# Kernel optimization log

Measured on AMD Instinct MI355X. Metric: run time of the kernel, lower is better.

Reference implementation:

```python
import jax, jax.numpy as jnp
import numpy as np

T = 1_000_000      # number of feature rows
D = 82             # STSIM feature dim (hardcoded Linear(82, 1))
NUM_GROUPS = 256   # N = mask.max() + 1 in the original (fixed for jit)


def setup_inputs() -> dict:
    key = jax.random.key(0)
    k1, k2, k3, k4, k5 = jax.random.split(key, 5)
    X1 = jax.random.normal(k1, (T, D), jnp.float32)
    X2 = jax.random.normal(k2, (T, D), jnp.float32)
    Y = jax.random.normal(k3, (T,), jnp.float32)
    mask = jax.random.randint(k4, (T,), 0, NUM_GROUPS)
    # Linear(82,1,bias=False) weight; positive (matches init_weight = 1/var)
    # so sqrt(M((X1-X2)^2)) is real.
    W = jax.random.uniform(k5, (1, D), jnp.float32, 0.01, 1.0)
    return {"X1": X1, "X2": X2, "Y": Y, "W": W, "mask": mask}


def _criterion(x, Y, mask):
    # Vectorized version of the per-group Pearson-correlation loop:
    # one pass of segment reductions instead of N full-array boolean masks.
    seg = lambda v: jax.ops.segment_sum(v, mask, num_segments=NUM_GROUPS)
    counts = seg(jnp.ones_like(x))                      # [N]
    xc = x - (seg(x) / counts)[mask]                    # per-group centered
    yc = Y - (seg(Y) / counts)[mask]
    nom = seg(xc * yc)                                  # [N]
    denom = jnp.sqrt(seg(xc * xc) * seg(yc * yc))       # [N]
    return jnp.sum(jnp.abs(nom / denom)) / NUM_GROUPS


def reference(X1, X2, Y, W, mask):
    # pred = sqrt(Linear((X1 - X2)^2))  -> [T, 1]
    pred = jnp.sqrt(((X1 - X2) ** 2) @ W.T)
    coeff = _criterion(pred[:, 0], Y, mask)
    return coeff, pred
```

## Files before the change

### kernel.cpp

```cpp
#include <hip/hip_runtime.h>
#include <hip/hip_bf16.h>

#define T_ROWS 1000000
#define D 82
#define NG 256

#define WS_CNT   0
#define WS_SUMP  256
#define WS_SUMY  512
#define WS_MEANP 768
#define WS_MEANY 1024
#define WS_SXY   1280
#define WS_SXX   1536
#define WS_SYY   1792
#define WS_FLOATS 2048

__global__ __launch_bounds__(256) void pred_kernel(
    const float* __restrict__ X1, const float* __restrict__ X2,
    const float* __restrict__ Y, const float* __restrict__ W,
    const int* __restrict__ mask, float* __restrict__ pred_out,
    float* __restrict__ ws)
{
    __shared__ float lds_w[D];
    __shared__ float lds_cnt[NG], lds_sp[NG], lds_sy[NG];
    const int t = threadIdx.x;
    if (t < D) lds_w[t] = W[t];
    lds_cnt[t] = 0.f; lds_sp[t] = 0.f; lds_sy[t] = 0.f;
    __syncthreads();

    const int pair = blockIdx.x * 256 + t;
    if (pair < T_ROWS / 2) {
        const float4* __restrict__ p1 = (const float4*)(X1 + (size_t)pair * (2 * D));
        const float4* __restrict__ p2 = (const float4*)(X2 + (size_t)pair * (2 * D));
        float accA = 0.f, accB = 0.f;
        #pragma unroll 5
        for (int k = 0; k < 20; ++k) {
            float4 a = p1[k], b = p2[k];
            float d;
            d = a.x - b.x; accA += d * d * lds_w[4 * k + 0];
            d = a.y - b.y; accA += d * d * lds_w[4 * k + 1];
            d = a.z - b.z; accA += d * d * lds_w[4 * k + 2];
            d = a.w - b.w; accA += d * d * lds_w[4 * k + 3];
        }
        {
            float4 a = p1[20], b = p2[20];
            float d;
            d = a.x - b.x; accA += d * d * lds_w[80];
            d = a.y - b.y; accA += d * d * lds_w[81];
            d = a.z - b.z; accB += d * d * lds_w[0];
            d = a.w - b.w; accB += d * d * lds_w[1];
        }
        #pragma unroll 5
        for (int k = 21; k < 41; ++k) {
            float4 a = p1[k], b = p2[k];
            const int c = 4 * k - 82;
            float d;
            d = a.x - b.x; accB += d * d * lds_w[c + 0];
            d = a.y - b.y; accB += d * d * lds_w[c + 1];
            d = a.z - b.z; accB += d * d * lds_w[c + 2];
            d = a.w - b.w; accB += d * d * lds_w[c + 3];
        }
        const float pA = sqrtf(accA);
        const float pB = sqrtf(accB);
        pred_out[2 * pair]     = pA;
        pred_out[2 * pair + 1] = pB;

        const int2   gg = *(const int2*)(mask + 2 * (size_t)pair);
        const float2 yy = *(const float2*)(Y + 2 * (size_t)pair);
        atomicAdd(&lds_cnt[gg.x], 1.f);  atomicAdd(&lds_cnt[gg.y], 1.f);
        atomicAdd(&lds_sp[gg.x], pA);    atomicAdd(&lds_sp[gg.y], pB);
        atomicAdd(&lds_sy[gg.x], yy.x);  atomicAdd(&lds_sy[gg.y], yy.y);
    }
    __syncthreads();
    atomicAdd(&ws[WS_CNT  + t], lds_cnt[t]);
    atomicAdd(&ws[WS_SUMP + t], lds_sp[t]);
    atomicAdd(&ws[WS_SUMY + t], lds_sy[t]);
}

__global__ void means_kernel(float* __restrict__ ws)
{
    const int g = threadIdx.x;
    const float c = ws[WS_CNT + g];
    ws[WS_MEANP + g] = ws[WS_SUMP + g] / c;
    ws[WS_MEANY + g] = ws[WS_SUMY + g] / c;
}

__global__ __launch_bounds__(256) void corr_kernel(
    const float* __restrict__ pred, const float* __restrict__ Y,
    const int* __restrict__ mask, float* __restrict__ ws)
{
    __shared__ float mP[NG], mY[NG], sxy[NG], sxx[NG], syy[NG];
    const int t = threadIdx.x;
    mP[t] = ws[WS_MEANP + t];
    mY[t] = ws[WS_MEANY + t];
    sxy[t] = 0.f; sxx[t] = 0.f; syy[t] = 0.f;
    __syncthreads();

    const int stride = gridDim.x * blockDim.x;
    for (int r = blockIdx.x * blockDim.x + t; r < T_ROWS; r += stride) {
        const int g = mask[r];
        const float xc = pred[r] - mP[g];
        const float yc = Y[r]    - mY[g];
        atomicAdd(&sxy[g], xc * yc);
        atomicAdd(&sxx[g], xc * xc);
        atomicAdd(&syy[g], yc * yc);
    }
    __syncthreads();
    atomicAdd(&ws[WS_SXY + t], sxy[t]);
    atomicAdd(&ws[WS_SXX + t], sxx[t]);
    atomicAdd(&ws[WS_SYY + t], syy[t]);
}

__global__ void final_kernel(const float* __restrict__ ws, float* __restrict__ out)
{
    __shared__ float red[NG];
    const int g = threadIdx.x;
    const float r = ws[WS_SXY + g] / sqrtf(ws[WS_SXX + g] * ws[WS_SYY + g]);
    red[g] = fabsf(r);
    __syncthreads();
    for (int s = 128; s > 0; s >>= 1) {
        if (g < s) red[g] += red[g + s];
        __syncthreads();
    }
    if (g == 0) out[0] = red[0] / (float)NG;
}

extern "C" void kernel_launch(void* const* d_in, const int* in_sizes, int n_in,
                              void* d_out, int out_size, void* d_ws, size_t ws_size,
                              hipStream_t stream)
{
    const float* X1   = (const float*)d_in[0];
    const float* X2   = (const float*)d_in[1];
    const float* Y    = (const float*)d_in[2];
    const float* W    = (const float*)d_in[3];
    const int*   mask = (const int*)d_in[4];
    float* out = (float*)d_out;
    float* ws  = (float*)d_ws;

    hipMemsetAsync(ws, 0, WS_FLOATS * sizeof(float), stream);

    const int pairs = T_ROWS / 2;
    const int gridA = (pairs + 255) / 256;
    pred_kernel<<<gridA, 256, 0, stream>>>(X1, X2, Y, W, mask, out + 1, ws);
    means_kernel<<<1, 256, 0, stream>>>(ws);
    corr_kernel<<<1024, 256, 0, stream>>>(out + 1, Y, mask, ws);
    final_kernel<<<1, 256, 0, stream>>>(ws, out);
}
```

Before: 723.2 us.

## Fuse prediction and correlation into one pass using raw-moment sums

Replaces the two-pass centered correlation (pred, means, corr kernels) with a single fused kernel that accumulates count, sums, cross-products and squares per group. The final kernel computes the correlation from these raw moments in double. The fused kernel stages a 64-row tile of X1-X2 differences in LDS with coalesced float4 loads and splits each row's dot product across 4 threads. It removes a kernel launch and the second read of pred, Y and mask. In exchange it issues per-row global atomics with no LDS pre-aggregation, which could contend heavily on 256 groups, and the float raw-moment accumulation risks cancellation error.

```diff
diff --git a/kernel.cpp b/kernel.cpp
--- a/kernel.cpp
+++ b/kernel.cpp
@@ -4,119 +4,91 @@
 #define T_ROWS 1000000
 #define D 82
 #define NG 256
+#define ROWS_PER_BLOCK 64
+#define TILE_FLOATS (ROWS_PER_BLOCK * D)
+#define TILE_F4     (TILE_FLOATS / 4)
 
-#define WS_CNT   0
-#define WS_SUMP  256
-#define WS_SUMY  512
-#define WS_MEANP 768
-#define WS_MEANY 1024
-#define WS_SXY   1280
-#define WS_SXX   1536
-#define WS_SYY   1792
-#define WS_FLOATS 2048
+#define WS_CNT 0
+#define WS_SX  256
+#define WS_SY  512
+#define WS_SXY 768
+#define WS_SXX 1024
+#define WS_SYY 1280
+#define WS_FLOATS 1536
 
-__global__ __launch_bounds__(256) void pred_kernel(
+__global__ __launch_bounds__(256) void fused_kernel(
     const float* __restrict__ X1, const float* __restrict__ X2,
     const float* __restrict__ Y, const float* __restrict__ W,
     const int* __restrict__ mask, float* __restrict__ pred_out,
     float* __restrict__ ws)
 {
-    __shared__ float lds_w[D];
-    __shared__ float lds_cnt[NG], lds_sp[NG], lds_sy[NG];
+    __shared__ float s_diff[TILE_FLOATS];
+    __shared__ float s_w[D];
+    __shared__ float s_part[4][ROWS_PER_BLOCK];
+
     const int t = threadIdx.x;
-    if (t < D) lds_w[t] = W[t];
-    lds_cnt[t] = 0.f; lds_sp[t] = 0.f; lds_sy[t] = 0.f;
+    const size_t r0 = (size_t)blockIdx.x * ROWS_PER_BLOCK;
+    const size_t base = r0 * D;
+
+    const float4* __restrict__ a4 = (const float4*)(X1 + base);
+    const float4* __restrict__ b4 = (const float4*)(X2 + base);
+    float4* s4 = (float4*)s_diff;
+
+    for (int i = t; i < TILE_F4; i += 256) {
+        float4 a = a4[i];
+        float4 b = b4[i];
+        float4 d;
+        d.x = a.x - b.x; d.y = a.y - b.y; d.z = a.z - b.z; d.w = a.w - b.w;
+        s4[i] = d;
+    }
+    if (t < D) s_w[t] = W[t];
     __syncthreads();
 
-    const int pair = blockIdx.x * 256 + t;
-    if (pair < T_ROWS / 2) {
-        const float4* __restrict__ p1 = (const float4*)(X1 + (size_t)pair * (2 * D));
-        const float4* __restrict__ p2 = (const float4*)(X2 + (size_t)pair * (2 * D));
-        float accA = 0.f, accB = 0.f;
-        #pragma unroll 5
-        for (int k = 0; k < 20; ++k) {
-            float4 a = p1[k], b = p2[k];
-            float d;
-            d = a.x - b.x; accA += d * d * lds_w[4 * k + 0];
-            d = a.y - b.y; accA += d * d * lds_w[4 * k + 1];
-            d = a.z - b.z; accA += d * d * lds_w[4 * k + 2];
-            d = a.w - b.w; accA += d * d * lds_w[4 * k + 3];
-        }
-        {
-            float4 a = p1[20], b = p2[20];
-            float d;
-            d = a.x - b.x; accA += d * d * lds_w[80];
-            d = a.y - b.y; accA += d * d * lds_w[81];
-            d = a.z - b.z; accB += d * d * lds_w[0];
-            d = a.w - b.w; accB += d * d * lds_w[1];
-        }
-        #pragma unroll 5
-        for (int k = 21; k < 41; ++k) {
-            float4 a = p1[k], b = p2[k];
-            const int c = 4 * k - 82;
-            float d;
-            d = a.x - b.x; accB += d * d * lds_w[c + 0];
-            d = a.y - b.y; accB += d * d * lds_w[c + 1];
-            d = a.z - b.z; accB += d * d * lds_w[c + 2];
-            d = a.w - b.w; accB += d * d * lds_w[c + 3];
-        }
-        const float pA = sqrtf(accA);
-        const float pB = sqrtf(accB);
-        pred_out[2 * pair]     = pA;
-        pred_out[2 * pair + 1] = pB;
-
-        const int2   gg = *(const int2*)(mask + 2 * (size_t)pair);
-        const float2 yy = *(const float2*)(Y + 2 * (size_t)pair);
-        atomicAdd(&lds_cnt[gg.x], 1.f);  atomicAdd(&lds_cnt[gg.y], 1.f);
-        atomicAdd(&lds_sp[gg.x], pA);    atomicAdd(&lds_sp[gg.y], pB);
-        atomicAdd(&lds_sy[gg.x], yy.x);  atomicAdd(&lds_sy[gg.y], yy.y);
+    const int q = t >> 6;
+    const int row = t & 63;
+    const int start = (q < 2) ? q * 21 : 42 + (q - 2) * 20;
+    const int len = (q < 2) ? 21 : 20;
+    const float* __restrict__ dr = s_diff + row * D;
+    float acc = 0.f;
+    #pragma unroll 7
+    for (int j = 0; j < len; ++j) {
+        const int k = start + j;
+        const float d = dr[k];
+        acc += d * d * s_w[k];
     }
-    __syncthreads();
-    atomicAdd(&ws[WS_CNT  + t], lds_cnt[t]);
-    atomicAdd(&ws[WS_SUMP + t], lds_sp[t]);
-    atomicAdd(&ws[WS_SUMY + t], lds_sy[t]);
-}
-
-__global__ void means_kernel(float* __restrict__ ws)
-{
-    const int g = threadIdx.x;
-    const float c = ws[WS_CNT + g];
-    ws[WS_MEANP + g] = ws[WS_SUMP + g] / c;
-    ws[WS_MEANY + g] = ws[WS_SUMY + g] / c;
-}
-
-__global__ __launch_bounds__(256) void corr_kernel(
-    const float* __restrict__ pred, const float* __restrict__ Y,
-    const int* __restrict__ mask, float* __restrict__ ws)
-{
-    __shared__ float mP[NG], mY[NG], sxy[NG], sxx[NG], syy[NG];
-    const int t = threadIdx.x;
-    mP[t] = ws[WS_MEANP + t];
-    mY[t] = ws[WS_MEANY + t];
-    sxy[t] = 0.f; sxx[t] = 0.f; syy[t] = 0.f;
+    s_part[q][row] = acc;
     __syncthreads();
 
-    const int stride = gridDim.x * blockDim.x;
-    for (int r = blockIdx.x * blockDim.x + t; r < T_ROWS; r += stride) {
-        const int g = mask[r];
-        const float xc = pred[r] - mP[g];
-        const float yc = Y[r]    - mY[g];
-        atomicAdd(&sxy[g], xc * yc);
-        atomicAdd(&sxx[g], xc * xc);
-        atomicAdd(&syy[g], yc * yc);
+    if (t < ROWS_PER_BLOCK) {
+        const float s = s_part[0][t] + s_part[1][t] + s_part[2][t] + s_part[3][t];
+        const float p = sqrtf(s);
+        pred_out[r0 + t] = p;
+
+        const int g = mask[r0 + t];
+        const float y = Y[r0 + t];
+        atomicAdd(&ws[WS_CNT + g], 1.0f);
+        atomicAdd(&ws[WS_SX  + g], p);
+        atomicAdd(&ws[WS_SY  + g], y);
+        atomicAdd(&ws[WS_SXY + g], p * y);
+        atomicAdd(&ws[WS_SXX + g], p * p);
+        atomicAdd(&ws[WS_SYY + g], y * y);
     }
-    __syncthreads();
-    atomicAdd(&ws[WS_SXY + t], sxy[t]);
-    atomicAdd(&ws[WS_SXX + t], sxx[t]);
-    atomicAdd(&ws[WS_SYY + t], syy[t]);
 }
 
 __global__ void final_kernel(const float* __restrict__ ws, float* __restrict__ out)
 {
     __shared__ float red[NG];
     const int g = threadIdx.x;
-    const float r = ws[WS_SXY + g] / sqrtf(ws[WS_SXX + g] * ws[WS_SYY + g]);
-    red[g] = fabsf(r);
+    const double n   = (double)ws[WS_CNT + g];
+    const double sx  = (double)ws[WS_SX  + g];
+    const double sy  = (double)ws[WS_SY  + g];
+    const double sxy = (double)ws[WS_SXY + g];
+    const double sxx = (double)ws[WS_SXX + g];
+    const double syy = (double)ws[WS_SYY + g];
+    const double num  = n * sxy - sx * sy;
+    const double varx = n * sxx - sx * sx;
+    const double vary = n * syy - sy * sy;
+    red[g] = (float)fabs(num / sqrt(varx * vary));
     __syncthreads();
     for (int s = 128; s > 0; s >>= 1) {
         if (g < s) red[g] += red[g + s];
@@ -139,10 +111,7 @@
 
     hipMemsetAsync(ws, 0, WS_FLOATS * sizeof(float), stream);
 
-    const int pairs = T_ROWS / 2;
-    const int gridA = (pairs + 255) / 256;
-    pred_kernel<<<gridA, 256, 0, stream>>>(X1, X2, Y, W, mask, out + 1, ws);
-    means_kernel<<<1, 256, 0, stream>>>(ws);
-    corr_kernel<<<1024, 256, 0, stream>>>(out + 1, Y, mask, ws);
-    final_kernel<<<1, 256, 0, stream>>>(ws, out);
+    const int grid = T_ROWS / ROWS_PER_BLOCK;
+    fused_kernel<<<grid, 256, 0, stream>>>(X1, X2, Y, W, mask, out + 1, ws);
+    final_kernel<<<1, NG, 0, stream>>>(ws, out);
 }
```

New measurement: 1.069 ms. 47.9% more time.
